# Optimization experiments

Hardware: AMD Instinct MI355X
Metric: run time of the kernel (lower is better)

## Reference

```python
import jax, jax.numpy as jnp
import numpy as np

NUM_HEADS = 20
MAX_SEQLEN = 1500  # max per-segment length (Whisper 30s -> 1500 frames); static for jit
NEG = -1e30


def setup_inputs() -> dict:
    key = jax.random.key(0)
    ks = jax.random.split(key, 6)
    B, S, D = 4, MAX_SEQLEN, 1280
    T = B * S
    hidden_states = jax.random.normal(ks[0], (T, D), dtype=jnp.float32)
    # packed varlen layout: 4 equal-length audio segments
    cu_seqlens = (jnp.arange(B + 1, dtype=jnp.int32) * S)
    w = 0.02
    Wq = jax.random.normal(ks[1], (D, D), dtype=jnp.float32) * w
    Wk = jax.random.normal(ks[2], (D, D), dtype=jnp.float32) * w
    Wv = jax.random.normal(ks[3], (D, D), dtype=jnp.float32) * w
    Wo = jax.random.normal(ks[4], (D, D), dtype=jnp.float32) * w
    bq = jnp.zeros((D,), jnp.float32)
    bv = jnp.zeros((D,), jnp.float32)
    bo = jnp.zeros((D,), jnp.float32)
    return {"hidden_states": hidden_states, "cu_seqlens": cu_seqlens,
            "Wq": Wq, "bq": bq, "Wk": Wk, "Wv": Wv, "bv": bv, "Wo": Wo, "bo": bo}


def _varlen_attention(hidden_states, cu_seqlens, Wq, bq, Wk, Wv, bv, Wo, bo):
    T, D = hidden_states.shape
    H = NUM_HEADS
    d = D // H
    scale = d ** -0.5
    S = MAX_SEQLEN
    B = cu_seqlens.shape[0] - 1

    # projections (torch nn.Linear convention: y = x @ W.T + b; k_proj has no bias)
    q = hidden_states @ Wq.T + bq   # [T, D]
    k = hidden_states @ Wk.T        # [T, D]
    v = hidden_states @ Wv.T + bv   # [T, D]

    lens = cu_seqlens[1:] - cu_seqlens[:-1]                 # [B]
    pos = jnp.arange(S, dtype=jnp.int32)                    # [S]
    valid = pos[None, :] < lens[:, None]                    # [B, S]
    idx = cu_seqlens[:-1, None] + pos[None, :]              # [B, S]
    idx_g = jnp.where(valid, idx, 0)

    # unpack to padded [B, S, H, d]
    qb = q[idx_g].reshape(B, S, H, d)
    kb = k[idx_g].reshape(B, S, H, d)
    vb = v[idx_g].reshape(B, S, H, d)

    scores = jnp.einsum('bqhd,bkhd->bhqk', qb, kb) * scale  # [B, H, S, S]
    scores = jnp.where(valid[:, None, None, :], scores, NEG)
    attn = jax.nn.softmax(scores, axis=-1)
    out = jnp.einsum('bhqk,bkhd->bqhd', attn, vb).reshape(B, S, D)

    # repack to [T, D]; invalid slots scatter out-of-bounds and are dropped
    idx_s = jnp.where(valid, idx, T).reshape(-1)
    packed = jnp.zeros((T, D), out.dtype).at[idx_s].set(out.reshape(-1, D), mode='drop')
    return packed @ Wo.T + bo


def reference(hidden_states, cu_seqlens, Wq, bq, Wk, Wv, bv, Wo, bo):
    return _varlen_attention(hidden_states, cu_seqlens, Wq, bq, Wk, Wv, bv, Wo, bo)
```

## Files before the change

kernel.cpp:

```cpp
#include <hip/hip_runtime.h>
#include <stdint.h>
#include <math.h>

#define DMODEL 1280
#define NHEAD  20
#define DHEAD  64
#define NSEG   4
#define MAXS   1500
#define SPAD   1536
#define TPAD   (NSEG*SPAD)
#define QT256  ((MAXS + 255) / 256)
#define BM 128
#define BN 128
#define BK 32
#define QSCALE 0.18033688011112042f
#define NEGV  -1e30f

typedef float  f32x4  __attribute__((ext_vector_type(4)));
typedef __bf16 bf16x8 __attribute__((ext_vector_type(8)));

#if __has_builtin(__builtin_amdgcn_exp2f)
#define EXP2F(x) __builtin_amdgcn_exp2f(x)
#else
#define EXP2F(x) exp2f(x)
#endif

__device__ __forceinline__ ushort f2bf(float f) {
  union { float f; uint32_t u; } a; a.f = f;
  uint32_t u = a.u;
  u += 0x7FFFu + ((u >> 16) & 1u);
  return (ushort)(u >> 16);
}

__device__ __forceinline__ uint32_t pk2(float a, float b) {
  union { float f; uint32_t u; } ua, ub; ua.f = a; ub.f = b;
  uint32_t x = ua.u + 0x8000u, y = ub.u + 0x8000u;
  return (x >> 16) | (y & 0xFFFF0000u);
}

__device__ __forceinline__ void async16(const void* g, void* lds) {
  __builtin_amdgcn_global_load_lds((const __attribute__((address_space(1))) void*)g,
                                   (__attribute__((address_space(3))) void*)lds,
                                   16, 0, 0);
}

__device__ __forceinline__ int perm32(int a) {
  return ((a >> 2) & 3) * 8 + ((a >> 4) & 1) * 4 + (a & 3);
}

__global__ void __launch_bounds__(256)
cvt_all(const float* __restrict__ hs, const float* __restrict__ Wq,
        const float* __restrict__ Wk, const float* __restrict__ Wv,
        const float* __restrict__ Wo, ushort* __restrict__ dst, int nX, int DD) {
  const int i = (blockIdx.x * 256 + threadIdx.x) * 4;
  const float* src;
  if (i < nX) {
    src = hs + i;
  } else {
    int j = i - nX;
    const int z = (j >= DD) + (j >= 2 * DD) + (j >= 3 * DD);
    const float* w = (z == 0) ? Wq : (z == 1) ? Wk : (z == 2) ? Wv : Wo;
    src = w + (j - z * DD);
  }
  float4 v = *(const float4*)src;
  ushort4 o;
  o.x = f2bf(v.x); o.y = f2bf(v.y); o.z = f2bf(v.z); o.w = f2bf(v.w);
  *(ushort4*)(dst + i) = o;
}

__device__ __forceinline__ void gemm_tile_mainloop(
    const ushort* __restrict__ A, const ushort* __restrict__ W,
    int M, int m0, int n0, ushort* As, ushort* Bs, f32x4 (&acc)[4][4])
{
  const int tid  = threadIdx.x;
  const int wave = tid >> 6, lane = tid & 63;
  const int quad = lane >> 4, c16 = lane & 15;
  const int wr = (wave >> 1) * 64, wc = (wave & 1) * 64;

  const int M0 = wave * 128 + lane, M1 = M0 + 64;
  const int sr0 = M0 >> 3, pp0 = M0 & 7, p0 = pp0 ^ (sr0 & 7);
  const int sr1 = M1 >> 3, pp1 = M1 & 7, p1 = pp1 ^ (sr1 & 7);
  const int row0 = sr0 * 2 + (p0 >> 2), kc0 = (p0 & 3) << 3;
  const int row1 = sr1 * 2 + (p1 >> 2), kc1 = (p1 & 3) << 3;
  const ushort* Ap0 = A + (size_t)(m0 + row0) * DMODEL + kc0;
  const ushort* Ap1 = A + (size_t)(m0 + row1) * DMODEL + kc1;
  const ushort* Bp0 = W + (size_t)(n0 + row0) * DMODEL + kc0;
  const ushort* Bp1 = W + (size_t)(n0 + row1) * DMODEL + kc1;
  const int o0 = wave * 1024;
  const int o1 = wave * 1024 + 512;
  const int BUF = BM * BK;

  async16(Ap0, As + o0); async16(Ap1, As + o1);
  async16(Bp0, Bs + o0); async16(Bp1, Bs + o1);

  int c = 0;
  for (int k0 = 0; k0 < DMODEL; k0 += BK, c ^= 1) {
    __syncthreads();
    if (k0 + BK < DMODEL) {
      const int kn = k0 + BK;
      const int bo = (c ^ 1) * BUF;
      async16(Ap0 + kn, As + bo + o0); async16(Ap1 + kn, As + bo + o1);
      async16(Bp0 + kn, Bs + bo + o0); async16(Bp1 + kn, Bs + bo + o1);
    }
    const ushort* Ab = As + c * BUF;
    const ushort* Bb = Bs + c * BUF;
    bf16x8 a[4], b[4];
#pragma unroll
    for (int i = 0; i < 4; ++i) {
      const int row = wr + i * 16 + c16;
      const int sr = row >> 1;
      const int off = (sr << 6) + (((((row & 1) << 2) | quad) ^ (sr & 7)) << 3);
      a[i] = *(const bf16x8*)(Ab + off);
    }
#pragma unroll
    for (int j = 0; j < 4; ++j) {
      const int row = wc + j * 16 + c16;
      const int sr = row >> 1;
      const int off = (sr << 6) + (((((row & 1) << 2) | quad) ^ (sr & 7)) << 3);
      b[j] = *(const bf16x8*)(Bb + off);
    }
#pragma unroll
    for (int i = 0; i < 4; ++i)
#pragma unroll
      for (int j = 0; j < 4; ++j)
        acc[i][j] = __builtin_amdgcn_mfma_f32_16x16x32_bf16(a[i], b[j], acc[i][j], 0, 0, 0);
  }
}

__global__ void __launch_bounds__(256, 4)
gemm_qkv(const ushort* __restrict__ X, const ushort* __restrict__ W4,
         const float* __restrict__ bq, const float* __restrict__ bv,
         const int* __restrict__ cu,
         ushort* __restrict__ qb, ushort* __restrict__ kb, ushort* __restrict__ vt, int M)
{
  __shared__ ushort As[2 * BM * BK], Bs[2 * BN * BK];
  const int wg = blockIdx.x;
  if (wg >= 30) return;
  const int z = wg / 10;
  const int n0 = (wg % 10) * BN;
  const int m0 = blockIdx.y * BM;
  const ushort* W = W4 + (size_t)z * DMODEL * DMODEL;

  f32x4 acc[4][4];
  f32x4 zero = {0.f, 0.f, 0.f, 0.f};
#pragma unroll
  for (int i = 0; i < 4; ++i)
#pragma unroll
    for (int j = 0; j < 4; ++j) acc[i][j] = zero;

  gemm_tile_mainloop(X, W, M, m0, n0, As, Bs, acc);

  const int tid = threadIdx.x, wave = tid >> 6, lane = tid & 63;
  const int quad = lane >> 4, c16 = lane & 15;
  const int wr = (wave >> 1) * 64, wc = (wave & 1) * 64;

  if (z == 2) {
    const int c1 = cu[1], c2 = cu[2], c3 = cu[3];
#pragma unroll
    for (int i = 0; i < 4; ++i) {
      const int t0 = m0 + wr + i * 16 + quad * 4;
      const int s0a = (t0 >= c1) + (t0 >= c2) + (t0 >= c3);
      const int s3a = (t0 + 3 >= c1) + (t0 + 3 >= c2) + (t0 + 3 >= c3);
      const int seg0 = (s0a == 0) ? 0 : (s0a == 1) ? c1 : (s0a == 2) ? c2 : c3;
#pragma unroll
      for (int j = 0; j < 4; ++j) {
        const int cfeat = n0 + wc + j * 16 + c16;
        const float bb = bv[cfeat];
        if (t0 + 3 < M && s0a == s3a) {
          const int s = t0 - seg0;
          const size_t base = (size_t)cfeat * TPAD + (size_t)s0a * SPAD
                            + (size_t)(s & ~31) + perm32(s & 31);
          ushort4 w;
          w.x = f2bf(acc[i][j][0] + bb);
          w.y = f2bf(acc[i][j][1] + bb);
          w.z = f2bf(acc[i][j][2] + bb);
          w.w = f2bf(acc[i][j][3] + bb);
          *(ushort4*)(vt + base) = w;
        } else {
#pragma unroll
          for (int r = 0; r < 4; ++r) {
            const int t = t0 + r;
            if (t < M) {
              const int sb = (t >= c1) + (t >= c2) + (t >= c3);
              const int sg = (sb == 0) ? 0 : (sb == 1) ? c1 : (sb == 2) ? c2 : c3;
              const int s = t - sg;
              vt[(size_t)cfeat * TPAD + (size_t)sb * SPAD + (s & ~31) + perm32(s & 31)]
                  = f2bf(acc[i][j][r] + bb);
            }
          }
        }
      }
    }
  } else {
    ushort* out = (z == 0) ? qb : kb;
    const float* bias = (z == 0) ? bq : (const float*)nullptr;
    const float oscale = (z == 0) ? QSCALE : 1.0f;
#pragma unroll
    for (int i = 0; i < 4; ++i) {
      const int rbase = m0 + wr + i * 16 + quad * 4;
#pragma unroll
      for (int j = 0; j < 4; ++j) {
        const int c = n0 + wc + j * 16 + c16;
        const float bb = bias ? bias[c] : 0.f;
#pragma unroll
        for (int r = 0; r < 4; ++r) {
          const int rr = rbase + r;
          if (rr < M) out[(size_t)rr * DMODEL + c] = f2bf((acc[i][j][r] + bb) * oscale);
        }
      }
    }
  }
}

__global__ void __launch_bounds__(256, 4)
gemm_out(const ushort* __restrict__ A, const ushort* __restrict__ W,
         const float* __restrict__ bias, float* __restrict__ out, int M)
{
  __shared__ ushort As[2 * BM * BK], Bs[2 * BN * BK];
  const int wg = blockIdx.x;
  if (wg >= 10) return;
  const int n0 = wg * BN;
  const int m0 = blockIdx.y * BM;
  f32x4 acc[4][4];
  f32x4 zero = {0.f, 0.f, 0.f, 0.f};
#pragma unroll
  for (int i = 0; i < 4; ++i)
#pragma unroll
    for (int j = 0; j < 4; ++j) acc[i][j] = zero;

  gemm_tile_mainloop(A, W, M, m0, n0, As, Bs, acc);

  const int tid = threadIdx.x, wave = tid >> 6, lane = tid & 63;
  const int quad = lane >> 4, c16 = lane & 15;
  const int wr = (wave >> 1) * 64, wc = (wave & 1) * 64;
#pragma unroll
  for (int i = 0; i < 4; ++i) {
    const int rbase = m0 + wr + i * 16 + quad * 4;
#pragma unroll
    for (int j = 0; j < 4; ++j) {
      const int c = n0 + wc + j * 16 + c16;
      const float bb = bias[c];
#pragma unroll
      for (int r = 0; r < 4; ++r) {
        const int rr = rbase + r;
        if (rr < M) out[(size_t)rr * DMODEL + c] = acc[i][j][r] + bb;
      }
    }
  }
}

__global__ void __launch_bounds__(512, 4)
attn_fused(const ushort* __restrict__ qb, const ushort* __restrict__ kb,
           const ushort* __restrict__ vt, ushort* __restrict__ ob,
           const int* __restrict__ cu, int T)
{
  __shared__ ushort SB[16384];
  const int hs = blockIdx.x;
  const int b = hs / NHEAD, h = hs % NHEAD;
  const int seg0 = cu[b];
  const int len  = cu[b + 1] - seg0;
  const int q0 = blockIdx.y * 256;
  if (q0 >= len) return;
  const int tid = threadIdx.x, wave = tid >> 6, lane = tid & 63;
  const int quad = lane >> 4, c16 = lane & 15;

#pragma unroll
  for (int t = 0; t < 4; ++t) {
    const int slot = t * 512 + tid;
    const int r = slot >> 3, k2 = slot & 7;
    const int col = ((k2 ^ (r & 7)) << 3);
    async16(qb + (size_t)(seg0 + q0 + r) * DMODEL + h * DHEAD + col,
            &SB[(t * 512 + wave * 64) * 8]);
  }

  const int rK = tid >> 3, kK = tid & 7;
  const int colK = ((kK ^ (rK & 7)) << 3);
  const ushort* kp = kb + (size_t)(seg0 + rK) * DMODEL + h * DHEAD + colK;
  const ushort* vp = vt + (size_t)(h * DHEAD + rK) * TPAD + (size_t)b * SPAD + colK;
  const int ldsoff = wave * 512;

  __syncthreads();

  bf16x8 aq[2][2];
#pragma unroll
  for (int n = 0; n < 2; ++n)
#pragma unroll
    for (int ks = 0; ks < 2; ++ks) {
      const int row = wave * 32 + n * 16 + c16;
      aq[n][ks] = *(const bf16x8*)(&SB[row * 64 + (((ks * 4 + quad) ^ (c16 & 7)) << 3)]);
    }

  __syncthreads();

  async16(kp, &SB[ldsoff]); async16(vp, &SB[4096 + ldsoff]);
  kp += (size_t)64 * DMODEL; vp += 64;

  float l_i[2] = {0.f, 0.f};
  f32x4 o_acc[2][4];
  f32x4 zero = {0.f, 0.f, 0.f, 0.f};
#pragma unroll
  for (int n = 0; n < 2; ++n)
#pragma unroll
    for (int m = 0; m < 4; ++m) o_acc[n][m] = zero;

  const int niter = (len + 63) >> 6;
  for (int it = 0; it < niter; ++it) {
    __syncthreads();
    const ushort* Kt = &SB[(it & 1) * 8192];
    const ushort* Vt = Kt + 4096;

    if (it + 1 < niter) {
      ushort* Dst = &SB[((it + 1) & 1) * 8192];
      async16(kp, Dst + ldsoff); async16(vp, Dst + 4096 + ldsoff);
      kp += (size_t)64 * DMODEL; vp += 64;
    }

    f32x4 s[2][4];
    __builtin_amdgcn_s_setprio(1);
#pragma unroll
    for (int f = 0; f < 4; ++f) {
      const int row = f * 16 + c16;
      const int ch = c16 & 7;
      bf16x8 ak0 = *(const bf16x8*)(Kt + row * 64 + ((quad ^ ch) << 3));
      bf16x8 ak1 = *(const bf16x8*)(Kt + row * 64 + (((4 + quad) ^ ch) << 3));
#pragma unroll
      for (int n = 0; n < 2; ++n) {
        s[n][f] = zero;
        s[n][f] = __builtin_amdgcn_mfma_f32_16x16x32_bf16(ak0, aq[n][0], s[n][f], 0, 0, 0);
        s[n][f] = __builtin_amdgcn_mfma_f32_16x16x32_bf16(ak1, aq[n][1], s[n][f], 0, 0, 0);
      }
    }
    __builtin_amdgcn_s_setprio(0);

    const int kv0 = it * 64;
    if (kv0 + 64 > len) {
#pragma unroll
      for (int f = 0; f < 4; ++f) {
        const int kvb = kv0 + f * 16 + quad * 4;
#pragma unroll
        for (int r = 0; r < 4; ++r)
          if (kvb + r >= len) { s[0][f][r] = NEGV; s[1][f][r] = NEGV; }
      }
    }

#pragma unroll
    for (int n = 0; n < 2; ++n) {
      float rs = 0.f;
#pragma unroll
      for (int f = 0; f < 4; ++f)
#pragma unroll
        for (int r = 0; r < 4; ++r) {
          const float p = EXP2F(s[n][f][r]);
          s[n][f][r] = p;
          rs += p;
        }
      l_i[n] += rs;
    }

    bf16x8 bp[2][2];
#pragma unroll
    for (int n = 0; n < 2; ++n)
#pragma unroll
      for (int g = 0; g < 2; ++g) {
        union { uint32_t u[4]; bf16x8 v; } cv;
        cv.u[0] = pk2(s[n][2 * g][0], s[n][2 * g][1]);
        cv.u[1] = pk2(s[n][2 * g][2], s[n][2 * g][3]);
        cv.u[2] = pk2(s[n][2 * g + 1][0], s[n][2 * g + 1][1]);
        cv.u[3] = pk2(s[n][2 * g + 1][2], s[n][2 * g + 1][3]);
        bp[n][g] = cv.v;
      }

    __builtin_amdgcn_s_setprio(1);
#pragma unroll
    for (int m = 0; m < 4; ++m) {
      const int row = m * 16 + c16;
      const int ch = c16 & 7;
      bf16x8 av0 = *(const bf16x8*)(Vt + row * 64 + ((quad ^ ch) << 3));
      bf16x8 av1 = *(const bf16x8*)(Vt + row * 64 + (((4 + quad) ^ ch) << 3));
#pragma unroll
      for (int n = 0; n < 2; ++n) {
        o_acc[n][m] = __builtin_amdgcn_mfma_f32_16x16x32_bf16(av0, bp[n][0], o_acc[n][m], 0, 0, 0);
        o_acc[n][m] = __builtin_amdgcn_mfma_f32_16x16x32_bf16(av1, bp[n][1], o_acc[n][m], 0, 0, 0);
      }
    }
    __builtin_amdgcn_s_setprio(0);
  }

#pragma unroll
  for (int n = 0; n < 2; ++n) {
    float l = l_i[n];
    l += __shfl_xor(l, 16);
    l += __shfl_xor(l, 32);
    const int q = q0 + wave * 32 + n * 16 + c16;
    if (q < len) {
      const float inv = 1.0f / l;
      const size_t base = (size_t)(seg0 + q) * DMODEL + h * DHEAD;
#pragma unroll
      for (int m = 0; m < 4; ++m) {
        ushort4 pk;
        pk.x = f2bf(o_acc[n][m][0] * inv);
        pk.y = f2bf(o_acc[n][m][1] * inv);
        pk.z = f2bf(o_acc[n][m][2] * inv);
        pk.w = f2bf(o_acc[n][m][3] * inv);
        *(ushort4*)(ob + base + m * 16 + quad * 4) = pk;
      }
    }
  }
}

extern "C" void kernel_launch(void* const* d_in, const int* in_sizes, int n_in,
                              void* d_out, int out_size, void* d_ws, size_t ws_size,
                              hipStream_t stream)
{
  (void)n_in; (void)out_size; (void)ws_size;
  const float* hs = (const float*)d_in[0];
  const int*   cu = (const int*)d_in[1];
  const float* Wq = (const float*)d_in[2];
  const float* bq = (const float*)d_in[3];
  const float* Wk = (const float*)d_in[4];
  const float* Wv = (const float*)d_in[5];
  const float* bv = (const float*)d_in[6];
  const float* Wo = (const float*)d_in[7];
  const float* bo = (const float*)d_in[8];
  float* out = (float*)d_out;
  const int T  = in_sizes[0] / DMODEL;
  const int DD = DMODEL * DMODEL;
  const int nX = T * DMODEL;

  ushort* ws  = (ushort*)d_ws;
  ushort* X   = ws;
  ushort* W4  = X + (size_t)nX;
  ushort* qb  = W4 + 4 * (size_t)DD;
  ushort* kb  = qb + (size_t)T * DMODEL;
  ushort* vt  = kb + (size_t)T * DMODEL;
  ushort* ob  = X;

  const int ncvt = nX + 4 * DD;
  cvt_all<<<(ncvt / 4 + 255) / 256, 256, 0, stream>>>(hs, Wq, Wk, Wv, Wo, ws, nX, DD);

  gemm_qkv<<<dim3(32, (T + BM - 1) / BM), 256, 0, stream>>>(
      X, W4, bq, bv, cu, qb, kb, vt, T);

  attn_fused<<<dim3(NSEG * NHEAD, QT256), 512, 0, stream>>>(qb, kb, vt, ob, cu, T);

  gemm_out<<<dim3(16, (T + BM - 1) / BM), 256, 0, stream>>>(
      ob, W4 + 3 * (size_t)DD, bo, out, T);
}
```

Measured before the change: 303.3 us.

## Triple-buffer GEMM mainloop, split QKV into three launches, use native bf16 casts

The shared GEMM mainloop goes from double to triple buffering, prefetching two K-tiles ahead, and replaces __syncthreads with an explicit vmcnt wait plus s_barrier. The QKV projection is split into three separate launches with exact grids, so the idle padded blocks (32 and 16 wide grids) go away. The output GEMM grid is trimmed the same way. In attention, the P-matrix bf16 packing now uses native __bf16 conversion instead of manual rounding. Triple buffering raises LDS use per block, which can limit occupancy, and the extra launches add overhead.

```diff
diff --git a/kernel.cpp b/kernel.cpp
--- a/kernel.cpp
+++ b/kernel.cpp
@@ -32,12 +32,6 @@
   return (ushort)(u >> 16);
 }
 
-__device__ __forceinline__ uint32_t pk2(float a, float b) {
-  union { float f; uint32_t u; } ua, ub; ua.f = a; ub.f = b;
-  uint32_t x = ua.u + 0x8000u, y = ub.u + 0x8000u;
-  return (x >> 16) | (y & 0xFFFF0000u);
-}
-
 __device__ __forceinline__ void async16(const void* g, void* lds) {
   __builtin_amdgcn_global_load_lds((const __attribute__((address_space(1))) void*)g,
                                    (__attribute__((address_space(3))) void*)lds,
@@ -47,6 +41,10 @@
 __device__ __forceinline__ int perm32(int a) {
   return ((a >> 2) & 3) * 8 + ((a >> 4) & 1) * 4 + (a & 3);
 }
+
+#define GBAR()  do { asm volatile("" ::: "memory"); __builtin_amdgcn_s_barrier(); \
+                     asm volatile("" ::: "memory"); } while (0)
+#define WAITV(n) asm volatile("s_waitcnt vmcnt(" #n ")" ::: "memory")
 
 __global__ void __launch_bounds__(256)
 cvt_all(const float* __restrict__ hs, const float* __restrict__ Wq,
@@ -92,13 +90,18 @@
 
   async16(Ap0, As + o0); async16(Ap1, As + o1);
   async16(Bp0, Bs + o0); async16(Bp1, Bs + o1);
+  async16(Ap0 + BK, As + BUF + o0); async16(Ap1 + BK, As + BUF + o1);
+  async16(Bp0 + BK, Bs + BUF + o0); async16(Bp1 + BK, Bs + BUF + o1);
 
   int c = 0;
-  for (int k0 = 0; k0 < DMODEL; k0 += BK, c ^= 1) {
-    __syncthreads();
-    if (k0 + BK < DMODEL) {
-      const int kn = k0 + BK;
-      const int bo = (c ^ 1) * BUF;
+  for (int k0 = 0; k0 < DMODEL; k0 += BK) {
+    if (k0 + BK < DMODEL) { WAITV(4); }
+    else                  { WAITV(0); }
+    GBAR();
+    const int kn = k0 + 2 * BK;
+    if (kn < DMODEL) {
+      int c2 = c + 2; if (c2 >= 3) c2 -= 3;
+      const int bo = c2 * BUF;
       async16(Ap0 + kn, As + bo + o0); async16(Ap1 + kn, As + bo + o1);
       async16(Bp0 + kn, Bs + bo + o0); async16(Bp1 + kn, Bs + bo + o1);
     }
@@ -124,22 +127,18 @@
 #pragma unroll
       for (int j = 0; j < 4; ++j)
         acc[i][j] = __builtin_amdgcn_mfma_f32_16x16x32_bf16(a[i], b[j], acc[i][j], 0, 0, 0);
+    c = (c == 2) ? 0 : c + 1;
   }
 }
 
 __global__ void __launch_bounds__(256, 4)
-gemm_qkv(const ushort* __restrict__ X, const ushort* __restrict__ W4,
-         const float* __restrict__ bq, const float* __restrict__ bv,
-         const int* __restrict__ cu,
-         ushort* __restrict__ qb, ushort* __restrict__ kb, ushort* __restrict__ vt, int M)
+gemm_proj(const ushort* __restrict__ X, const ushort* __restrict__ W,
+          const float* __restrict__ bias, const int* __restrict__ cu,
+          ushort* __restrict__ out, int M, int mode)
 {
-  __shared__ ushort As[2 * BM * BK], Bs[2 * BN * BK];
-  const int wg = blockIdx.x;
-  if (wg >= 30) return;
-  const int z = wg / 10;
-  const int n0 = (wg % 10) * BN;
+  __shared__ ushort As[3 * BM * BK], Bs[3 * BN * BK];
+  const int n0 = blockIdx.x * BN;
   const int m0 = blockIdx.y * BM;
-  const ushort* W = W4 + (size_t)z * DMODEL * DMODEL;
 
   f32x4 acc[4][4];
   f32x4 zero = {0.f, 0.f, 0.f, 0.f};
@@ -154,7 +153,7 @@
   const int quad = lane >> 4, c16 = lane & 15;
   const int wr = (wave >> 1) * 64, wc = (wave & 1) * 64;
 
-  if (z == 2) {
+  if (mode == 2) {
     const int c1 = cu[1], c2 = cu[2], c3 = cu[3];
 #pragma unroll
     for (int i = 0; i < 4; ++i) {
@@ -165,7 +164,7 @@
 #pragma unroll
       for (int j = 0; j < 4; ++j) {
         const int cfeat = n0 + wc + j * 16 + c16;
-        const float bb = bv[cfeat];
+        const float bb = bias[cfeat];
         if (t0 + 3 < M && s0a == s3a) {
           const int s = t0 - seg0;
           const size_t base = (size_t)cfeat * TPAD + (size_t)s0a * SPAD
@@ -175,7 +174,7 @@
           w.y = f2bf(acc[i][j][1] + bb);
           w.z = f2bf(acc[i][j][2] + bb);
           w.w = f2bf(acc[i][j][3] + bb);
-          *(ushort4*)(vt + base) = w;
+          *(ushort4*)(out + base) = w;
         } else {
 #pragma unroll
           for (int r = 0; r < 4; ++r) {
@@ -184,7 +183,7 @@
               const int sb = (t >= c1) + (t >= c2) + (t >= c3);
               const int sg = (sb == 0) ? 0 : (sb == 1) ? c1 : (sb == 2) ? c2 : c3;
               const int s = t - sg;
-              vt[(size_t)cfeat * TPAD + (size_t)sb * SPAD + (s & ~31) + perm32(s & 31)]
+              out[(size_t)cfeat * TPAD + (size_t)sb * SPAD + (s & ~31) + perm32(s & 31)]
                   = f2bf(acc[i][j][r] + bb);
             }
           }
@@ -192,16 +191,14 @@
       }
     }
   } else {
-    ushort* out = (z == 0) ? qb : kb;
-    const float* bias = (z == 0) ? bq : (const float*)nullptr;
-    const float oscale = (z == 0) ? QSCALE : 1.0f;
+    const float oscale = (mode == 0) ? QSCALE : 1.0f;
 #pragma unroll
     for (int i = 0; i < 4; ++i) {
       const int rbase = m0 + wr + i * 16 + quad * 4;
 #pragma unroll
       for (int j = 0; j < 4; ++j) {
         const int c = n0 + wc + j * 16 + c16;
-        const float bb = bias ? bias[c] : 0.f;
+        const float bb = (mode == 0) ? bias[c] : 0.f;
 #pragma unroll
         for (int r = 0; r < 4; ++r) {
           const int rr = rbase + r;
@@ -216,10 +213,8 @@
 gemm_out(const ushort* __restrict__ A, const ushort* __restrict__ W,
          const float* __restrict__ bias, float* __restrict__ out, int M)
 {
-  __shared__ ushort As[2 * BM * BK], Bs[2 * BN * BK];
-  const int wg = blockIdx.x;
-  if (wg >= 10) return;
-  const int n0 = wg * BN;
+  __shared__ ushort As[3 * BM * BK], Bs[3 * BN * BK];
+  const int n0 = blockIdx.x * BN;
   const int m0 = blockIdx.y * BM;
   f32x4 acc[4][4];
   f32x4 zero = {0.f, 0.f, 0.f, 0.f};
@@ -362,12 +357,13 @@
     for (int n = 0; n < 2; ++n)
 #pragma unroll
       for (int g = 0; g < 2; ++g) {
-        union { uint32_t u[4]; bf16x8 v; } cv;
-        cv.u[0] = pk2(s[n][2 * g][0], s[n][2 * g][1]);
-        cv.u[1] = pk2(s[n][2 * g][2], s[n][2 * g][3]);
-        cv.u[2] = pk2(s[n][2 * g + 1][0], s[n][2 * g + 1][1]);
-        cv.u[3] = pk2(s[n][2 * g + 1][2], s[n][2 * g + 1][3]);
-        bp[n][g] = cv.v;
+        bf16x8 t;
+#pragma unroll
+        for (int r = 0; r < 4; ++r) {
+          t[r]     = (__bf16)s[n][2 * g][r];
+          t[r + 4] = (__bf16)s[n][2 * g + 1][r];
+        }
+        bp[n][g] = t;
       }
 
     __builtin_amdgcn_s_setprio(1);
@@ -438,11 +434,12 @@
   const int ncvt = nX + 4 * DD;
   cvt_all<<<(ncvt / 4 + 255) / 256, 256, 0, stream>>>(hs, Wq, Wk, Wv, Wo, ws, nX, DD);
 
-  gemm_qkv<<<dim3(32, (T + BM - 1) / BM), 256, 0, stream>>>(
-      X, W4, bq, bv, cu, qb, kb, vt, T);
+  const dim3 gproj(10, (T + BM - 1) / BM);
+  gemm_proj<<<gproj, 256, 0, stream>>>(X, W4,                    bq, cu, qb, T, 0);
+  gemm_proj<<<gproj, 256, 0, stream>>>(X, W4 + (size_t)DD,  nullptr, cu, kb, T, 1);
+  gemm_proj<<<gproj, 256, 0, stream>>>(X, W4 + 2 * (size_t)DD,   bv, cu, vt, T, 2);
 
   attn_fused<<<dim3(NSEG * NHEAD, QT256), 512, 0, stream>>>(qb, kb, vt, ob, cu, T);
 
-  gemm_out<<<dim3(16, (T + BM - 1) / BM), 256, 0, stream>>>(
-      ob, W4 + 3 * (size_t)DD, bo, out, T);
-}
+  gemm_out<<<gproj, 256, 0, stream>>>(ob, W4 + 3 * (size_t)DD, bo, out, T);
+}
```

Result: slower. 316.8 us (+4.5%).
